# Kernel tuning notes

Hardware: AMD Instinct MI355X
Metric: run time of the kernel (lower is better)

## Reference

```python
import jax, jax.numpy as jnp
import numpy as np

IN_CH_IMG = 256
CHANNELS = 256
NUM_CLASSES = 1
NUM_LAYERS = 4  # NUM_FC=3 -> 4 layers
IN_CH = IN_CH_IMG + 256  # pos-enc adds 256 channels
N_INST = 128
N_PTS = 2048

W_SIZES = [IN_CH * CHANNELS, CHANNELS * CHANNELS, CHANNELS * CHANNELS, CHANNELS * NUM_CLASSES]
B_SIZES = [CHANNELS, CHANNELS, CHANNELS, NUM_CLASSES]
NUM_PARAMS = sum(W_SIZES) + sum(B_SIZES)  # 263169


def setup_inputs() -> dict:
    key = jax.random.key(0)
    k1, k2, k3, k4 = jax.random.split(key, 4)
    return {
        "fine_grained_features": jax.random.normal(k1, (N_INST, IN_CH_IMG, N_PTS), dtype=jnp.float32),
        "point_coords": jax.random.uniform(k2, (N_INST, N_PTS, 2), dtype=jnp.float32),
        "parameters": jax.random.normal(k3, (N_INST, NUM_PARAMS), dtype=jnp.float32) * 0.05,
        "pe_gaussian": jax.random.normal(k4, (2, 128), dtype=jnp.float32),
    }


def _parse_params(params):
    # params: [N, NUM_PARAMS]. Weight blocks first, then bias blocks.
    n = params.shape[0]
    out_dims = [CHANNELS, CHANNELS, CHANNELS, NUM_CLASSES]
    in_dims = [IN_CH, CHANNELS, CHANNELS, CHANNELS]
    weights, biases = [], []
    off = 0
    for l in range(NUM_LAYERS):
        weights.append(params[:, off:off + W_SIZES[l]].reshape(n, out_dims[l], in_dims[l]))
        off += W_SIZES[l]
    for l in range(NUM_LAYERS):
        biases.append(params[:, off:off + B_SIZES[l]].reshape(n, out_dims[l], 1))
        off += B_SIZES[l]
    return weights, biases


def reference(fine_grained_features, point_coords, parameters, pe_gaussian):
    n, _, p = fine_grained_features.shape
    # Positional encoding: [N*P, 2] -> [N*P, 128] -> sin/cos -> [N, 256, P]
    loc = (2.0 * point_coords.reshape(n * p, 2) - 1.0) @ pe_gaussian
    loc = 2.0 * np.pi * loc
    pe = jnp.concatenate([jnp.sin(loc), jnp.cos(loc)], axis=1)  # [N*P, 256]
    pe = pe.reshape(n, p, 256).transpose(0, 2, 1)  # [N, 256, P]
    x = jnp.concatenate([pe, fine_grained_features], axis=1)  # [N, IN_CH, P]

    weights, biases = _parse_params(parameters)
    for i, (w, b) in enumerate(zip(weights, biases)):
        x = jnp.einsum('nck,ndc->ndk', x, w) + b
        if i < NUM_LAYERS - 1:
            x = jax.nn.relu(x)
    return x.reshape(-1, NUM_CLASSES, p)  # [N, 1, P]
```

## Files before the change

kernel.cpp:

```cpp
#include <hip/hip_runtime.h>
#include <hip/hip_fp16.h>


#define NI      128
#define NPTS    2048
#define CH      256
#define NPARAM  263169
#define PT      64
#define NTILES  (NPTS / PT)
#define ROWS    536

#define WOFF0   0
#define WOFF1   131072
#define WOFF2   196608
#define WOFF3   262144
#define BOFF0   262400
#define BOFF1   262656
#define BOFF2   262912
#define BOFF3   263168

#define PI_L0   0
#define PI_L1   131072
#define PI_L2   196608
#define PI_L3   262144
#define WS_PER_INST 262400
#define WS_BYTES ((size_t)NI * WS_PER_INST * 2)

typedef __fp16   h16x2 __attribute__((ext_vector_type(2)));
typedef _Float16 f16x8 __attribute__((ext_vector_type(8)));
typedef float    f32x4 __attribute__((ext_vector_type(4)));

union pack8 { h16x2 h[4]; f16x8 v; };

__global__ __launch_bounds__(256) void iph_prep(
    const float* __restrict__ params, _Float16* __restrict__ wsw)
{
    const int inst = blockIdx.y;
    const int r = blockIdx.x * 256 + threadIdx.x;
    if (r >= 32800) return;
    const float* __restrict__ P = params + (size_t)inst * NPARAM;
    _Float16* __restrict__ W = wsw + (size_t)inst * WS_PER_INST;

    int rl, woff, K, dst;
    if (r < 16384)      { rl = r;         woff = WOFF0; K = 512; dst = PI_L0; }
    else if (r < 24576) { rl = r - 16384; woff = WOFF1; K = 256; dst = PI_L1; }
    else if (r < 32768) { rl = r - 24576; woff = WOFF2; K = 256; dst = PI_L2; }
    else {
        const int e = (r - 32768) * 8;
        f16x8 v;
        #pragma unroll
        for (int j = 0; j < 8; ++j) v[j] = (_Float16)P[WOFF3 + e + j];
        *(f16x8*)&W[PI_L3 + e] = v;
        return;
    }
    const int e    = rl * 8;
    const int lane = rl & 63;
    const int cb   = (rl >> 6) & 15;
    const int ks   = rl >> 10;
    const int co   = (cb >> 1) * 32 + 2 * (lane & 15) + (cb & 1);
    const int k    = ks * 32 + (lane >> 4) * 8;
    const float* __restrict__ src = P + woff + co * K + k;
    f16x8 v;
    #pragma unroll
    for (int j = 0; j < 8; ++j) v[j] = (_Float16)src[j];
    *(f16x8*)&W[dst + e] = v;
}

template<bool PREPPED>
__global__ __launch_bounds__(512, 4) void iph_main(
    const float* __restrict__ feat,
    const float* __restrict__ coords,
    const float* __restrict__ params,
    const _Float16* __restrict__ wsw,
    const float* __restrict__ peg,
    float* __restrict__ out)
{
    __shared__ _Float16 X[PT * ROWS];

    const int bid  = blockIdx.x;
    const int inst = (bid & 7) | ((bid >> 8) << 3);
    const int tile = (bid >> 3) & 31;
    const int p0   = tile * PT;
    const int tid  = threadIdx.x;
    const int lane = tid & 63;
    const int wave = tid >> 6;
    const int l15  = lane & 15;
    const int hi   = lane >> 4;
    const float* __restrict__ P = params + (size_t)inst * NPARAM;
    const _Float16* __restrict__ WI = wsw + (size_t)inst * WS_PER_INST;

    {
        const int pt   = tid >> 3;
        const int part = tid & 7;
        const float2 cc = *(const float2*)&coords[((size_t)inst * NPTS + p0 + pt) * 2];
        const float a = 2.f * cc.x - 1.f;
        const float b = 2.f * cc.y - 1.f;
        float sv[16], cv[16];
        #pragma unroll
        for (int j = 0; j < 16; ++j) {
            const int f = part * 16 + j;
            float locr = a * peg[f] + b * peg[128 + f];
            locr -= floorf(locr);
            sv[j] = __builtin_amdgcn_sinf(locr);
            cv[j] = __builtin_amdgcn_cosf(locr);
        }
        pack8 s0, s1, c0, c1;
        #pragma unroll
        for (int q = 0; q < 4; ++q) {
            s0.h[q] = __builtin_amdgcn_cvt_pkrtz(sv[2*q],     sv[2*q + 1]);
            s1.h[q] = __builtin_amdgcn_cvt_pkrtz(sv[8 + 2*q], sv[9 + 2*q]);
            c0.h[q] = __builtin_amdgcn_cvt_pkrtz(cv[2*q],     cv[2*q + 1]);
            c1.h[q] = __builtin_amdgcn_cvt_pkrtz(cv[8 + 2*q], cv[9 + 2*q]);
        }
        _Float16* base = &X[pt * ROWS + part * 16];
        *(f16x8*)(base)           = s0.v;
        *(f16x8*)(base + 8)       = s1.v;
        *(f16x8*)(base + 128)     = c0.v;
        *(f16x8*)(base + 136)     = c1.v;
    }
    {
        const float* fbase = feat + (size_t)inst * CH * NPTS + p0 + lane;
        #pragma unroll
        for (int s = 0; s < 4; ++s) {
            const int c0i = s * 64 + wave * 8;
            float w8[8];
            #pragma unroll
            for (int j = 0; j < 8; ++j)
                w8[j] = fbase[(size_t)(c0i + j) * NPTS];
            pack8 pk;
            #pragma unroll
            for (int q = 0; q < 4; ++q)
                pk.h[q] = __builtin_amdgcn_cvt_pkrtz(w8[2*q], w8[2*q + 1]);
            *(f16x8*)&X[lane * ROWS + 256 + c0i] = pk.v;
        }
    }
    __syncthreads();

    auto run_layer = [&](const int foff, const int woff, const int boff, const int K) {
        f32x4 acc[4][2];
        #pragma unroll
        for (int mt = 0; mt < 4; ++mt)
            #pragma unroll
            for (int nt = 0; nt < 2; ++nt)
                acc[mt][nt] = (f32x4){0.f, 0.f, 0.f, 0.f};

        const int nks = K >> 5;
        #pragma unroll 2
        for (int ks = 0; ks < nks; ++ks) {
            f16x8 bfrag[2];
            #pragma unroll
            for (int nt = 0; nt < 2; ++nt) {
                if (PREPPED) {
                    const int cb = wave * 2 + nt;
                    bfrag[nt] = *(const f16x8*)&WI[foff + (((ks * 16 + cb) * 64 + lane) << 3)];
                } else {
                    const int co = wave * 32 + 2 * l15 + nt;
                    const float* wp = P + woff + (size_t)co * K + ks * 32 + hi * 8;
                    float w8[8];
                    __builtin_memcpy(w8, wp, 32);
                    f16x8 bb;
                    #pragma unroll
                    for (int j = 0; j < 8; ++j) bb[j] = (_Float16)w8[j];
                    bfrag[nt] = bb;
                }
            }
            f16x8 afrag[4];
            #pragma unroll
            for (int mt = 0; mt < 4; ++mt)
                afrag[mt] = *(const f16x8*)&X[(mt * 16 + l15) * ROWS + ks * 32 + hi * 8];
            #pragma unroll
            for (int mt = 0; mt < 4; ++mt)
                #pragma unroll
                for (int nt = 0; nt < 2; ++nt)
                    acc[mt][nt] = __builtin_amdgcn_mfma_f32_16x16x32_f16(
                        afrag[mt], bfrag[nt], acc[mt][nt], 0, 0, 0);
        }

        const float2 bb = *(const float2*)&P[boff + wave * 32 + 2 * l15];

        __syncthreads();
        #pragma unroll
        for (int mt = 0; mt < 4; ++mt) {
            #pragma unroll
            for (int r = 0; r < 4; ++r) {
                const float v0 = fmaxf(acc[mt][0][r] + bb.x, 0.f);
                const float v1 = fmaxf(acc[mt][1][r] + bb.y, 0.f);
                const h16x2 e = __builtin_amdgcn_cvt_pkrtz(v0, v1);
                const int pt = mt * 16 + hi * 4 + r;
                *(h16x2*)&X[pt * ROWS + wave * 32 + 2 * l15] = e;
            }
        }
        __syncthreads();
    };

    run_layer(PI_L0, WOFF0, BOFF0, 512);
    run_layer(PI_L1, WOFF1, BOFF1, 256);
    run_layer(PI_L2, WOFF2, BOFF2, 256);

    {
        const int pt   = tid >> 3;
        const int part = tid & 7;
        float sum = 0.f;
        #pragma unroll
        for (int q = 0; q < 4; ++q) {
            const f16x8 v = *(const f16x8*)&X[pt * ROWS + part * 8 + q * 64];
            if (PREPPED) {
                const f16x8 w = *(const f16x8*)&WI[PI_L3 + part * 8 + q * 64];
                #pragma unroll
                for (int j = 0; j < 8; ++j) sum += (float)v[j] * (float)w[j];
            } else {
                const float* wp = P + WOFF3 + part * 8 + q * 64;
                float w8[8];
                __builtin_memcpy(w8, wp, 32);
                #pragma unroll
                for (int j = 0; j < 8; ++j) sum += (float)v[j] * w8[j];
            }
        }
        sum += __shfl_xor(sum, 1);
        sum += __shfl_xor(sum, 2);
        sum += __shfl_xor(sum, 4);
        if (part == 0)
            out[(size_t)inst * NPTS + p0 + pt] = sum + P[BOFF3];
    }
}

extern "C" void kernel_launch(void* const* d_in, const int* in_sizes, int n_in,
                              void* d_out, int out_size, void* d_ws, size_t ws_size,
                              hipStream_t stream) {
    (void)in_sizes; (void)n_in; (void)out_size;
    const float* feat   = (const float*)d_in[0];
    const float* coords = (const float*)d_in[1];
    const float* params = (const float*)d_in[2];
    const float* peg    = (const float*)d_in[3];
    float* out = (float*)d_out;

    dim3 grid(NI * NTILES);
    dim3 block(512);

    if (ws_size >= WS_BYTES) {
        _Float16* wsw = (_Float16*)d_ws;
        iph_prep<<<dim3(129, 128), dim3(256), 0, stream>>>(params, wsw);
        iph_main<true><<<grid, block, 0, stream>>>(feat, coords, params, wsw, peg, out);
    } else {
        iph_main<false><<<grid, block, 0, stream>>>(feat, coords, params,
                                                    (const _Float16*)d_ws, peg, out);
    }
}
```

Baseline: 242.9 us.

## Software-pipeline MFMA fragment loads and fuse final layer into layer-2 epilogue

Replaces the per-layer lambda with a templated GEMM tile that double-buffers A (LDS) and B (global) fragments one k-step ahead, and raises wave priority around MFMA bursts with s_setprio. The final 256->1 projection is now computed straight from the layer-2 accumulators in registers using shuffles and a small shared partial-sum array. This avoids writing layer-2 activations back to LDS and one extra barrier. It costs more registers for the prefetch buffers, which could cut occupancy under the launch bound of 4 blocks.

```diff
diff --git a/kernel.cpp b/kernel.cpp
--- a/kernel.cpp
+++ b/kernel.cpp
@@ -66,6 +66,98 @@
     *(f16x8*)&W[dst + e] = v;
 }
 
+template<int NKS, bool PREPPED>
+__device__ __forceinline__ void gemm_tile(
+    f32x4 (&acc)[4][2],
+    const _Float16* __restrict__ bsrc,
+    const float* __restrict__ pw,
+    const _Float16* __restrict__ X,
+    int lane, int wave, int l15, int hi)
+{
+    if constexpr (PREPPED) {
+        const _Float16* bp = bsrc + ((wave * 2) * 64 + lane) * 8;
+        const _Float16* ap = &X[l15 * ROWS + hi * 8];
+        f16x8 a0[4], a1[4], b0[2], b1[2];
+        #pragma unroll
+        for (int nt = 0; nt < 2; ++nt) {
+            b0[nt] = *(const f16x8*)(bp + nt * 512);
+            b1[nt] = *(const f16x8*)(bp + 8192 + nt * 512);
+        }
+        #pragma unroll
+        for (int mt = 0; mt < 4; ++mt)
+            a0[mt] = *(const f16x8*)(ap + mt * 16 * ROWS);
+
+        #pragma unroll
+        for (int ks = 0; ks < NKS; ks += 2) {
+            f16x8 b2[2], b3[2];
+            if (ks + 2 < NKS) {
+                #pragma unroll
+                for (int nt = 0; nt < 2; ++nt)
+                    b2[nt] = *(const f16x8*)(bp + (ks + 2) * 8192 + nt * 512);
+            }
+            #pragma unroll
+            for (int mt = 0; mt < 4; ++mt)
+                a1[mt] = *(const f16x8*)(ap + mt * 16 * ROWS + (ks + 1) * 32);
+
+            __builtin_amdgcn_s_setprio(1);
+            #pragma unroll
+            for (int mt = 0; mt < 4; ++mt) {
+                acc[mt][0] = __builtin_amdgcn_mfma_f32_16x16x32_f16(a0[mt], b0[0], acc[mt][0], 0, 0, 0);
+                acc[mt][1] = __builtin_amdgcn_mfma_f32_16x16x32_f16(a0[mt], b0[1], acc[mt][1], 0, 0, 0);
+            }
+            __builtin_amdgcn_s_setprio(0);
+
+            if (ks + 2 < NKS) {
+                #pragma unroll
+                for (int nt = 0; nt < 2; ++nt)
+                    b3[nt] = *(const f16x8*)(bp + (ks + 3) * 8192 + nt * 512);
+                #pragma unroll
+                for (int mt = 0; mt < 4; ++mt)
+                    a0[mt] = *(const f16x8*)(ap + mt * 16 * ROWS + (ks + 2) * 32);
+            }
+
+            __builtin_amdgcn_s_setprio(1);
+            #pragma unroll
+            for (int mt = 0; mt < 4; ++mt) {
+                acc[mt][0] = __builtin_amdgcn_mfma_f32_16x16x32_f16(a1[mt], b1[0], acc[mt][0], 0, 0, 0);
+                acc[mt][1] = __builtin_amdgcn_mfma_f32_16x16x32_f16(a1[mt], b1[1], acc[mt][1], 0, 0, 0);
+            }
+            __builtin_amdgcn_s_setprio(0);
+
+            if (ks + 2 < NKS) {
+                #pragma unroll
+                for (int nt = 0; nt < 2; ++nt) { b0[nt] = b2[nt]; b1[nt] = b3[nt]; }
+            }
+        }
+    } else {
+        const int K = NKS * 32;
+        for (int ks = 0; ks < NKS; ++ks) {
+            f16x8 bfrag[2];
+            #pragma unroll
+            for (int nt = 0; nt < 2; ++nt) {
+                const int co = wave * 32 + 2 * l15 + nt;
+                const float* wp = pw + (size_t)co * K + ks * 32 + hi * 8;
+                float w8[8];
+                __builtin_memcpy(w8, wp, 32);
+                f16x8 bb;
+                #pragma unroll
+                for (int j = 0; j < 8; ++j) bb[j] = (_Float16)w8[j];
+                bfrag[nt] = bb;
+            }
+            f16x8 afrag[4];
+            #pragma unroll
+            for (int mt = 0; mt < 4; ++mt)
+                afrag[mt] = *(const f16x8*)&X[(mt * 16 + l15) * ROWS + ks * 32 + hi * 8];
+            #pragma unroll
+            for (int mt = 0; mt < 4; ++mt)
+                #pragma unroll
+                for (int nt = 0; nt < 2; ++nt)
+                    acc[mt][nt] = __builtin_amdgcn_mfma_f32_16x16x32_f16(
+                        afrag[mt], bfrag[nt], acc[mt][nt], 0, 0, 0);
+        }
+    }
+}
+
 template<bool PREPPED>
 __global__ __launch_bounds__(512, 4) void iph_main(
     const float* __restrict__ feat,
@@ -76,6 +168,7 @@
     float* __restrict__ out)
 {
     __shared__ _Float16 X[PT * ROWS];
+    __shared__ float    partial[8][PT];
 
     const int bid  = blockIdx.x;
     const int inst = (bid & 7) | ((bid >> 8) << 3);
@@ -136,49 +229,7 @@
     }
     __syncthreads();
 
-    auto run_layer = [&](const int foff, const int woff, const int boff, const int K) {
-        f32x4 acc[4][2];
-        #pragma unroll
-        for (int mt = 0; mt < 4; ++mt)
-            #pragma unroll
-            for (int nt = 0; nt < 2; ++nt)
-                acc[mt][nt] = (f32x4){0.f, 0.f, 0.f, 0.f};
-
-        const int nks = K >> 5;
-        #pragma unroll 2
-        for (int ks = 0; ks < nks; ++ks) {
-            f16x8 bfrag[2];
-            #pragma unroll
-            for (int nt = 0; nt < 2; ++nt) {
-                if (PREPPED) {
-                    const int cb = wave * 2 + nt;
-                    bfrag[nt] = *(const f16x8*)&WI[foff + (((ks * 16 + cb) * 64 + lane) << 3)];
-                } else {
-                    const int co = wave * 32 + 2 * l15 + nt;
-                    const float* wp = P + woff + (size_t)co * K + ks * 32 + hi * 8;
-                    float w8[8];
-                    __builtin_memcpy(w8, wp, 32);
-                    f16x8 bb;
-                    #pragma unroll
-                    for (int j = 0; j < 8; ++j) bb[j] = (_Float16)w8[j];
-                    bfrag[nt] = bb;
-                }
-            }
-            f16x8 afrag[4];
-            #pragma unroll
-            for (int mt = 0; mt < 4; ++mt)
-                afrag[mt] = *(const f16x8*)&X[(mt * 16 + l15) * ROWS + ks * 32 + hi * 8];
-            #pragma unroll
-            for (int mt = 0; mt < 4; ++mt)
-                #pragma unroll
-                for (int nt = 0; nt < 2; ++nt)
-                    acc[mt][nt] = __builtin_amdgcn_mfma_f32_16x16x32_f16(
-                        afrag[mt], bfrag[nt], acc[mt][nt], 0, 0, 0);
-        }
-
-        const float2 bb = *(const float2*)&P[boff + wave * 32 + 2 * l15];
-
-        __syncthreads();
+    auto write_epilogue = [&](f32x4 (&acc)[4][2], const float2 bb) {
         #pragma unroll
         for (int mt = 0; mt < 4; ++mt) {
             #pragma unroll
@@ -190,37 +241,66 @@
                 *(h16x2*)&X[pt * ROWS + wave * 32 + 2 * l15] = e;
             }
         }
-        __syncthreads();
     };
 
-    run_layer(PI_L0, WOFF0, BOFF0, 512);
-    run_layer(PI_L1, WOFF1, BOFF1, 256);
-    run_layer(PI_L2, WOFF2, BOFF2, 256);
-
-    {
-        const int pt   = tid >> 3;
-        const int part = tid & 7;
-        float sum = 0.f;
-        #pragma unroll
-        for (int q = 0; q < 4; ++q) {
-            const f16x8 v = *(const f16x8*)&X[pt * ROWS + part * 8 + q * 64];
-            if (PREPPED) {
-                const f16x8 w = *(const f16x8*)&WI[PI_L3 + part * 8 + q * 64];
-                #pragma unroll
-                for (int j = 0; j < 8; ++j) sum += (float)v[j] * (float)w[j];
-            } else {
-                const float* wp = P + WOFF3 + part * 8 + q * 64;
-                float w8[8];
-                __builtin_memcpy(w8, wp, 32);
-                #pragma unroll
-                for (int j = 0; j < 8; ++j) sum += (float)v[j] * w8[j];
-            }
-        }
-        sum += __shfl_xor(sum, 1);
-        sum += __shfl_xor(sum, 2);
-        sum += __shfl_xor(sum, 4);
-        if (part == 0)
-            out[(size_t)inst * NPTS + p0 + pt] = sum + P[BOFF3];
+    {
+        f32x4 acc[4][2];
+        #pragma unroll
+        for (int mt = 0; mt < 4; ++mt)
+            #pragma unroll
+            for (int nt = 0; nt < 2; ++nt)
+                acc[mt][nt] = (f32x4){0.f, 0.f, 0.f, 0.f};
+        const float2 bb = *(const float2*)&P[BOFF0 + wave * 32 + 2 * l15];
+        gemm_tile<16, PREPPED>(acc, WI + PI_L0, P + WOFF0, X, lane, wave, l15, hi);
+        __syncthreads();
+        write_epilogue(acc, bb);
+        __syncthreads();
+    }
+    {
+        f32x4 acc[4][2];
+        #pragma unroll
+        for (int mt = 0; mt < 4; ++mt)
+            #pragma unroll
+            for (int nt = 0; nt < 2; ++nt)
+                acc[mt][nt] = (f32x4){0.f, 0.f, 0.f, 0.f};
+        const float2 bb = *(const float2*)&P[BOFF1 + wave * 32 + 2 * l15];
+        gemm_tile<8, PREPPED>(acc, WI + PI_L1, P + WOFF1, X, lane, wave, l15, hi);
+        __syncthreads();
+        write_epilogue(acc, bb);
+        __syncthreads();
+    }
+    {
+        f32x4 acc[4][2];
+        #pragma unroll
+        for (int mt = 0; mt < 4; ++mt)
+            #pragma unroll
+            for (int nt = 0; nt < 2; ++nt)
+                acc[mt][nt] = (f32x4){0.f, 0.f, 0.f, 0.f};
+        const float2 bb = *(const float2*)&P[BOFF2 + wave * 32 + 2 * l15];
+        const float2 w3 = *(const float2*)&P[WOFF3 + wave * 32 + 2 * l15];
+        gemm_tile<8, PREPPED>(acc, WI + PI_L2, P + WOFF2, X, lane, wave, l15, hi);
+        #pragma unroll
+        for (int mt = 0; mt < 4; ++mt) {
+            #pragma unroll
+            for (int r = 0; r < 4; ++r) {
+                const float v0 = fmaxf(acc[mt][0][r] + bb.x, 0.f);
+                const float v1 = fmaxf(acc[mt][1][r] + bb.y, 0.f);
+                float s = v0 * w3.x + v1 * w3.y;
+                s += __shfl_xor(s, 1);
+                s += __shfl_xor(s, 2);
+                s += __shfl_xor(s, 4);
+                s += __shfl_xor(s, 8);
+                if (l15 == 0)
+                    partial[wave][mt * 16 + hi * 4 + r] = s;
+            }
+        }
+        __syncthreads();
+        if (tid < PT) {
+            float s = P[BOFF3];
+            #pragma unroll
+            for (int w = 0; w < 8; ++w) s += partial[w][tid];
+            out[(size_t)inst * NPTS + p0 + tid] = s;
+        }
     }
 }
 
```

Result: faster. 217.3 us (-10.5%).
